# Kernel tuning notes

Measured on AMD Instinct MI355X. Metric: run time of the kernel, lower is better.

## Reference

```python
import jax, jax.numpy as jnp
import numpy as np
from math import factorial, sqrt

L = 8
RCUT = 5.0
PI = 3.14159  # literal used in the torch module's Ylm normalization
N_POINTS = 4194304


def powcmplx(zr, zi, n):
    # Faithful port, including the n>2 recurrence that uses the *updated*
    # real part when forming the imaginary part (as in the source).
    if n == 0:
        return jnp.ones_like(zr), jnp.zeros_like(zr)
    if n == 1:
        return zr, zi
    if n == 2:
        return zr * zr - zi * zi, 2.0 * zr * zi
    r, im = zr, zi
    for _ in range(2, n + 1):
        r = zr * r - zi * im
        im = zr * im + zi * r  # uses updated r, matching the source exactly
    return r, im


def _forward(pos):
    norms = jnp.sqrt(jnp.sum(pos * pos, axis=1))
    valid = norms > 0
    mask = valid.astype(pos.dtype)
    safe = jnp.where(valid, norms, 1.0)
    # cosine_cutoff uses the true pi (acos trick in the source)
    cut = 0.5 * (jnp.cos(norms * (jnp.pi / RCUT)) + 1.0)
    cut = jnp.where(norms > RCUT, 0.0, cut) * mask  # mask replaces boolean row-select
    xp_r = -0.5 * pos[:, 0]
    xp_i = -0.5 * pos[:, 1]
    xm_r = 0.5 * pos[:, 0]
    xm_i = -0.5 * pos[:, 1]
    x0 = pos[:, 2]
    n_out = (L + 1) ** 2
    vals = [jnp.zeros((), pos.dtype)] * n_out
    i = 0
    for l in range(L + 1):
        w_l = cut / safe ** l * sqrt((2 * l + 1) / 4 / PI)  # per-point weight for this l
        for M in range(-l, 1):
            m = abs(M)
            sr = jnp.zeros_like(x0)
            si = jnp.zeros_like(x0)
            for p in range(l + 1):
                q = p - m
                s = l - p - q
                if q >= 0 and s >= 0:
                    z1r, z1i = powcmplx(xp_r, xp_i, p)
                    z2r, z2i = powcmplx(xm_r, xm_i, q)
                    zr = z1r ** 2 - z2i ** 2      # faithful to source (squared terms)
                    zi = z1r * z2i + z1i * z2r
                    c = 1.0 / (factorial(p) * factorial(q) * factorial(s))
                    sr = sr + zr * x0 * c          # source multiplies by x0 (x0**s is unused there)
                    si = si + zi * x0 * c
            f = sqrt(factorial(l + m) * factorial(l - m))
            w = f * w_l
            clm_r = jnp.sum(sr * w)
            clm_i = jnp.sum(si * w)
            if m == 0:
                vals[i] = clm_r
            else:
                fac = sqrt(2.0) * (-1) ** m
                vals[i] = fac * clm_i
                vals[i + 2 * m] = fac * clm_r
            i += 1
        i += l
    return jnp.stack(vals).reshape(-1, 1)


def setup_inputs() -> dict:
    key = jax.random.key(0)
    pos = jax.random.normal(key, (N_POINTS, 3), dtype=jnp.float32) * 2.0
    return {"pos": pos}


def reference(pos):
    return _forward(pos)
```

## Files before the change

kernel.cpp:

```cpp
#include <hip/hip_runtime.h>
#include <math.h>


typedef float f32x2 __attribute__((ext_vector_type(2)));

#define NL 8
#define NACC 45
#define NBLK 1024
#define NTHR 256

__device__ __forceinline__ f32x2 pkfma(f32x2 a, f32x2 b, f32x2 c) {
    return __builtin_elementwise_fma(a, b, c);
}

__device__ __forceinline__ float waveReduce(float v) {
    v += __shfl_down(v, 32);
    v += __shfl_down(v, 16);
    v += __shfl_down(v, 8);
    v += __shfl_down(v, 4);
    v += __shfl_down(v, 2);
    v += __shfl_down(v, 1);
    return v;
}

__device__ __forceinline__ void point_body(float x, float y, float z,
                                           f32x2* __restrict__ accp) {
    const float FACT[9] = {1.f, 1.f, 2.f, 6.f, 24.f, 120.f, 720.f, 5040.f, 40320.f};

    const float r2 = x * x + y * y + z * z;
    const bool valid = r2 > 0.0f;
    const float inv0 = __builtin_amdgcn_rsqf(r2);
    const float norm = r2 * inv0;
    float cut = 0.5f * (__cosf(norm * 0.6283185307179586f) + 1.0f);
    cut = (r2 > 25.0f) ? 0.0f : cut;
    cut = valid ? cut : 0.0f;
    const float inv = valid ? inv0 : 1.0f;
    const float x0c = z * cut;

    const f32x2 w  = { -0.5f * x,  0.5f * x };
    const f32x2 wi = { -0.5f * y, -0.5f * y };

    f32x2 zr[9], zi[9];
    zr[0] = f32x2{1.f, 1.f}; zi[0] = f32x2{0.f, 0.f};
    zr[1] = w;               zi[1] = wi;
    zr[2] = w * w - wi * wi;
    zi[2] = (w + w) * wi;
    {
        f32x2 cr = zr[2];
        f32x2 ci = w * wi + wi * cr;
#pragma unroll
        for (int k = 3; k <= NL; ++k) {
            const f32x2 nr = w * cr - wi * ci;
            const f32x2 ni = w * ci + wi * nr;
            cr = nr; ci = ni;
            zr[k] = nr; zi[k] = ni;
        }
    }

    float aa[9], bb[9], cc[9], dd[9], sqa[9];
#pragma unroll
    for (int p = 0; p <= NL; ++p) {
        aa[p] = zr[p].x;
        cc[p] = zr[p].y;
        bb[p] = zi[p].x;
        dd[p] = zi[p].y;
        sqa[p] = aa[p] * aa[p];
    }

    float h[9];
    h[0] = x0c;
#pragma unroll
    for (int l = 1; l <= NL; ++l) h[l] = h[l - 1] * inv;

#pragma unroll
    for (int m = 0; m <= NL; ++m) {
        f32x2 Y[9];
#pragma unroll
        for (int p = 0; p <= NL; ++p) {
            if (p >= m && 2 * p - m <= NL) {
                const int q = p - m;
                const float cpq = 1.0f / (FACT[p] * FACT[q]);
                const float bc = bb[p] * cc[q];
                const f32x2 A = { -dd[q], aa[p] };
                const f32x2 B = {  dd[q], dd[q] };
                const f32x2 C = { sqa[p], bc };
                const f32x2 Yv = pkfma(A, B, C);
                Y[p] = Yv * f32x2{cpq, cpq};
            }
        }
#pragma unroll
        for (int l = m; l <= NL; ++l) {
            f32x2 s = {0.f, 0.f};
#pragma unroll
            for (int p = 0; p <= NL; ++p) {
                if (p >= m && 2 * p - m <= l) {
                    const int sidx = l - 2 * p + m;
                    const float is = 1.0f / FACT[sidx];
                    s = pkfma(Y[p], f32x2{is, is}, s);
                }
            }
            const int ai = l * (l + 1) / 2 + m;
            accp[ai] = pkfma(s, f32x2{h[l], h[l]}, accp[ai]);
        }
    }
}

__global__ __launch_bounds__(256, 2)
void sht_main(const float* __restrict__ pos, float* __restrict__ ws, int n) {
    f32x2 accp[NACC];
#pragma unroll
    for (int i = 0; i < NACC; ++i) accp[i] = f32x2{0.f, 0.f};

    const int t = blockIdx.x * NTHR + threadIdx.x;
    const int nthreads = NBLK * NTHR;
    const int nchunks = (n / 4 + nthreads - 1) / nthreads;

    for (int c = 0; c < nchunks; ++c) {
        const int idx = (c * nthreads + t) * 4;
        float xs[4], ys[4], zs[4];
        if (idx + 4 <= n) {
            const float4* p4 = reinterpret_cast<const float4*>(pos + (size_t)3 * idx);
            const float4 q0 = p4[0];
            const float4 q1 = p4[1];
            const float4 q2 = p4[2];
            xs[0] = q0.x; ys[0] = q0.y; zs[0] = q0.z;
            xs[1] = q0.w; ys[1] = q1.x; zs[1] = q1.y;
            xs[2] = q1.z; ys[2] = q1.w; zs[2] = q2.x;
            xs[3] = q2.y; ys[3] = q2.z; zs[3] = q2.w;
        } else {
#pragma unroll
            for (int k = 0; k < 4; ++k) {
                const int i = idx + k;
                const bool ok = i < n;
                xs[k] = ok ? pos[3 * i + 0] : 0.f;
                ys[k] = ok ? pos[3 * i + 1] : 0.f;
                zs[k] = ok ? pos[3 * i + 2] : 0.f;
            }
        }
#pragma unroll
        for (int k = 0; k < 4; ++k)
            point_body(xs[k], ys[k], zs[k], accp);
    }

    __shared__ float red[81][5];
    const int lane = threadIdx.x & 63;
    const int wave = threadIdx.x >> 6;

#pragma unroll
    for (int m = 0; m <= NL; ++m) {
#pragma unroll
        for (int l = m; l <= NL; ++l) {
            const int ai = l * (l + 1) / 2 + m;
            float vr = waveReduce(accp[ai].x);
            if (lane == 0) red[l * l + l + m][wave] = vr;
            if (m > 0) {
                float vi = waveReduce(accp[ai].y);
                if (lane == 0) red[l * l + l - m][wave] = vi;
            }
        }
    }
    __syncthreads();

    if ((int)threadIdx.x < 81) {
        float s = 0.f;
#pragma unroll
        for (int w = 0; w < 4; ++w) s += red[threadIdx.x][w];
        ws[(size_t)threadIdx.x * NBLK + blockIdx.x] = s;
    }
}

__device__ double dfact(int nn) {
    double r = 1.0;
    for (int i = 2; i <= nn; ++i) r *= (double)i;
    return r;
}

__global__ __launch_bounds__(256)
void sht_finalize(const float* __restrict__ ws, float* __restrict__ out) {
    const int j = blockIdx.x;
    const int t = threadIdx.x;
    float s = 0.f;
#pragma unroll
    for (int k = 0; k < NBLK / 256; ++k)
        s += ws[(size_t)j * NBLK + k * 256 + t];
    s = waveReduce(s);

    __shared__ float red[4];
    const int lane = t & 63, wave = t >> 6;
    if (lane == 0) red[wave] = s;
    __syncthreads();
    if (t == 0) {
        float tot = red[0] + red[1] + red[2] + red[3];
        int l = 0;
        while ((l + 1) * (l + 1) <= j) ++l;
        const int M = j - l * l - l;
        const int m = (M < 0) ? -M : M;
        double sc = sqrt(dfact(l + m) * dfact(l - m)) *
                    sqrt((double)(2 * l + 1) / (4.0 * 3.14159));
        if (m > 0) sc *= sqrt(2.0) * ((m & 1) ? -1.0 : 1.0);
        out[j] = (float)((double)tot * sc);
    }
}

extern "C" void kernel_launch(void* const* d_in, const int* in_sizes, int n_in,
                              void* d_out, int out_size, void* d_ws, size_t ws_size,
                              hipStream_t stream) {
    const float* pos = (const float*)d_in[0];
    const int npts = in_sizes[0] / 3;
    float* ws = (float*)d_ws;
    float* out = (float*)d_out;

    sht_main<<<NBLK, NTHR, 0, stream>>>(pos, ws, npts);
    sht_finalize<<<81, 256, 0, stream>>>(ws, out);
}
```

Before: 139.9 us.

## Pack two points per packed-FP32 lane instead of real/imag pairs

Restructures the per-point work so each f32x2 packed operation handles two different points, rather than the real and imaginary parts of one point. Accumulators are split into separate real and imaginary scalar arrays, and the two lanes are folded with scalar FMAs at accumulation time. The aim is fuller use of packed FP32 math, since the old layout wasted lanes on the m=0 terms and on the shuffles needed to build its operands. Launch bounds drop from 2 to 1 block per CU minimum, allowing more registers per thread at the cost of occupancy.

Measured after the change: 183.1 us. 30.9% more time.

```diff
diff --git a/kernel.cpp b/kernel.cpp
--- a/kernel.cpp
+++ b/kernel.cpp
@@ -9,9 +9,7 @@
 #define NBLK 1024
 #define NTHR 256
 
-__device__ __forceinline__ f32x2 pkfma(f32x2 a, f32x2 b, f32x2 c) {
-    return __builtin_elementwise_fma(a, b, c);
-}
+__device__ __forceinline__ f32x2 sp(float v) { return f32x2{v, v}; }
 
 __device__ __forceinline__ float waveReduce(float v) {
     v += __shfl_down(v, 32);
@@ -23,93 +21,110 @@
     return v;
 }
 
-__device__ __forceinline__ void point_body(float x, float y, float z,
-                                           f32x2* __restrict__ accp) {
+__device__ __forceinline__ void pair_body(
+    float xA, float yA, float zA,
+    float xB, float yB, float zB,
+    float* __restrict__ accr, float* __restrict__ acci)
+{
     const float FACT[9] = {1.f, 1.f, 2.f, 6.f, 24.f, 120.f, 720.f, 5040.f, 40320.f};
 
-    const float r2 = x * x + y * y + z * z;
-    const bool valid = r2 > 0.0f;
-    const float inv0 = __builtin_amdgcn_rsqf(r2);
-    const float norm = r2 * inv0;
-    float cut = 0.5f * (__cosf(norm * 0.6283185307179586f) + 1.0f);
-    cut = (r2 > 25.0f) ? 0.0f : cut;
-    cut = valid ? cut : 0.0f;
-    const float inv = valid ? inv0 : 1.0f;
-    const float x0c = z * cut;
-
-    const f32x2 w  = { -0.5f * x,  0.5f * x };
-    const f32x2 wi = { -0.5f * y, -0.5f * y };
-
-    f32x2 zr[9], zi[9];
-    zr[0] = f32x2{1.f, 1.f}; zi[0] = f32x2{0.f, 0.f};
-    zr[1] = w;               zi[1] = wi;
-    zr[2] = w * w - wi * wi;
-    zi[2] = (w + w) * wi;
+    float x0s[2], invsc[2];
+#pragma unroll
+    for (int k = 0; k < 2; ++k) {
+        const float x = k ? xB : xA;
+        const float y = k ? yB : yA;
+        const float z = k ? zB : zA;
+        const float r2 = x * x + y * y + z * z;
+        const bool valid = r2 > 0.0f;
+        const float inv0 = __builtin_amdgcn_rsqf(r2);
+        const float norm = r2 * inv0;
+        float cut = 0.5f * (__cosf(norm * 0.6283185307179586f) + 1.0f);
+        cut = (r2 > 25.0f) ? 0.0f : cut;
+        cut = valid ? cut : 0.0f;
+        invsc[k] = valid ? inv0 : 1.0f;
+        x0s[k] = z * cut;
+    }
+
+    const f32x2 invp = { invsc[0], invsc[1] };
+    f32x2 h[9];
+    h[0] = f32x2{ x0s[0], x0s[1] };
+#pragma unroll
+    for (int l = 1; l <= NL; ++l) h[l] = h[l - 1] * invp;
+
+    const f32x2 w1 = { -0.5f * xA, -0.5f * xB };
+    const f32x2 wi = { -0.5f * yA, -0.5f * yB };
+    const f32x2 w2 = {  0.5f * xA,  0.5f * xB };
+
+    f32x2 a[9], b[9], c[9], d[9];
+    a[0] = sp(1.f); b[0] = sp(0.f); c[0] = sp(1.f); d[0] = sp(0.f);
+    a[1] = w1;      b[1] = wi;      c[1] = w2;      d[1] = wi;
+    a[2] = w1 * w1 - wi * wi;  b[2] = (w1 + w1) * wi;
+    c[2] = w2 * w2 - wi * wi;  d[2] = (w2 + w2) * wi;
     {
-        f32x2 cr = zr[2];
-        f32x2 ci = w * wi + wi * cr;
+        f32x2 cr = a[2];
+        f32x2 ci = w1 * wi + wi * cr;
 #pragma unroll
         for (int k = 3; k <= NL; ++k) {
-            const f32x2 nr = w * cr - wi * ci;
-            const f32x2 ni = w * ci + wi * nr;
+            const f32x2 nr = w1 * cr - wi * ci;
+            const f32x2 ni = w1 * ci + wi * nr;
             cr = nr; ci = ni;
-            zr[k] = nr; zi[k] = ni;
-        }
-    }
-
-    float aa[9], bb[9], cc[9], dd[9], sqa[9];
-#pragma unroll
-    for (int p = 0; p <= NL; ++p) {
-        aa[p] = zr[p].x;
-        cc[p] = zr[p].y;
-        bb[p] = zi[p].x;
-        dd[p] = zi[p].y;
-        sqa[p] = aa[p] * aa[p];
-    }
-
-    float h[9];
-    h[0] = x0c;
-#pragma unroll
-    for (int l = 1; l <= NL; ++l) h[l] = h[l - 1] * inv;
+            a[k] = nr; b[k] = ni;
+        }
+    }
+    {
+        f32x2 cr = c[2];
+        f32x2 ci = w2 * wi + wi * cr;
+#pragma unroll
+        for (int k = 3; k <= NL; ++k) {
+            const f32x2 nr = w2 * cr - wi * ci;
+            const f32x2 ni = w2 * ci + wi * nr;
+            cr = nr; ci = ni;
+            c[k] = nr; d[k] = ni;
+        }
+    }
+
+    f32x2 sqa[9];
+#pragma unroll
+    for (int p = 0; p <= NL; ++p) sqa[p] = a[p] * a[p];
 
 #pragma unroll
     for (int m = 0; m <= NL; ++m) {
-        f32x2 Y[9];
+        f32x2 Yr[9], Yi[9];
 #pragma unroll
         for (int p = 0; p <= NL; ++p) {
             if (p >= m && 2 * p - m <= NL) {
                 const int q = p - m;
                 const float cpq = 1.0f / (FACT[p] * FACT[q]);
-                const float bc = bb[p] * cc[q];
-                const f32x2 A = { -dd[q], aa[p] };
-                const f32x2 B = {  dd[q], dd[q] };
-                const f32x2 C = { sqa[p], bc };
-                const f32x2 Yv = pkfma(A, B, C);
-                Y[p] = Yv * f32x2{cpq, cpq};
+                Yr[p] = (sqa[p] - d[q] * d[q]) * sp(cpq);
+                if (m > 0)
+                    Yi[p] = (a[p] * d[q] + b[p] * c[q]) * sp(cpq);
             }
         }
 #pragma unroll
         for (int l = m; l <= NL; ++l) {
-            f32x2 s = {0.f, 0.f};
+            f32x2 sr = sp(0.f), si = sp(0.f);
 #pragma unroll
             for (int p = 0; p <= NL; ++p) {
                 if (p >= m && 2 * p - m <= l) {
                     const int sidx = l - 2 * p + m;
                     const float is = 1.0f / FACT[sidx];
-                    s = pkfma(Y[p], f32x2{is, is}, s);
+                    sr += Yr[p] * sp(is);
+                    if (m > 0) si += Yi[p] * sp(is);
                 }
             }
             const int ai = l * (l + 1) / 2 + m;
-            accp[ai] = pkfma(s, f32x2{h[l], h[l]}, accp[ai]);
-        }
-    }
-}
-
-__global__ __launch_bounds__(256, 2)
+            accr[ai] = fmaf(sr.y, h[l].y, fmaf(sr.x, h[l].x, accr[ai]));
+            if (m > 0)
+                acci[ai] = fmaf(si.y, h[l].y, fmaf(si.x, h[l].x, acci[ai]));
+        }
+    }
+}
+
+__global__ __launch_bounds__(256, 1)
 void sht_main(const float* __restrict__ pos, float* __restrict__ ws, int n) {
-    f32x2 accp[NACC];
-#pragma unroll
-    for (int i = 0; i < NACC; ++i) accp[i] = f32x2{0.f, 0.f};
+    float accr[NACC], acci[NACC];
+#pragma unroll
+    for (int i = 0; i < NACC; ++i) { accr[i] = 0.f; acci[i] = 0.f; }
 
     const int t = blockIdx.x * NTHR + threadIdx.x;
     const int nthreads = NBLK * NTHR;
@@ -137,9 +152,8 @@
                 zs[k] = ok ? pos[3 * i + 2] : 0.f;
             }
         }
-#pragma unroll
-        for (int k = 0; k < 4; ++k)
-            point_body(xs[k], ys[k], zs[k], accp);
+        pair_body(xs[0], ys[0], zs[0], xs[1], ys[1], zs[1], accr, acci);
+        pair_body(xs[2], ys[2], zs[2], xs[3], ys[3], zs[3], accr, acci);
     }
 
     __shared__ float red[81][5];
@@ -151,10 +165,10 @@
 #pragma unroll
         for (int l = m; l <= NL; ++l) {
             const int ai = l * (l + 1) / 2 + m;
-            float vr = waveReduce(accp[ai].x);
+            float vr = waveReduce(accr[ai]);
             if (lane == 0) red[l * l + l + m][wave] = vr;
             if (m > 0) {
-                float vi = waveReduce(accp[ai].y);
+                float vi = waveReduce(acci[ai]);
                 if (lane == 0) red[l * l + l - m][wave] = vi;
             }
         }
```
